# Kernel tuning notes

Measured on AMD Instinct MI355X. Metric: run time of the kernel, lower is better.

The kernel has to match this reference:

```python
import jax, jax.numpy as jnp
import numpy as np

B, S, HID = 1, 2048, 4096
H, HKV = 32, 8
D = HID // H          # 128
G = H // HKV          # 4 query heads per kv head (GQA)


def setup_inputs() -> dict:
    key = jax.random.key(0)
    ks = jax.random.split(key, 5)
    hidden_states = jax.random.normal(ks[0], (B, S, HID), dtype=jnp.float32)
    # additive causal mask: 0 on/below diagonal, large negative above
    causal = jnp.tril(jnp.ones((S, S), dtype=bool))
    attention_mask = jnp.where(causal, 0.0, -1e9).astype(jnp.float32)[None, None]
    sc = 0.02
    wq = jax.random.normal(ks[1], (HID, H * D), dtype=jnp.float32) * sc
    wk = jax.random.normal(ks[2], (HID, HKV * D), dtype=jnp.float32) * sc
    wv = jax.random.normal(ks[3], (HID, HKV * D), dtype=jnp.float32) * sc
    wo = jax.random.normal(ks[4], (H * D, HID), dtype=jnp.float32) * sc
    return {"hidden_states": hidden_states, "attention_mask": attention_mask,
            "wq": wq, "wk": wk, "wv": wv, "wo": wo}


def reference(hidden_states, attention_mask, wq, wk, wv, wo):
    # projections (lora_rank=0 path: plain dense, no bias)
    q = hidden_states @ wq                      # [B,S,H*D]
    k = hidden_states @ wk                      # [B,S,HKV*D]
    v = hidden_states @ wv                      # [B,S,HKV*D]
    # split heads; group query heads by their kv head: head h -> (h//G, h%G)
    q = q.reshape(B, S, HKV, G, D).transpose(0, 2, 3, 1, 4)   # [B,HKV,G,S,D]
    k = k.reshape(B, S, HKV, D).transpose(0, 2, 1, 3)          # [B,HKV,S,D]
    v = v.reshape(B, S, HKV, D).transpose(0, 2, 1, 3)          # [B,HKV,S,D]
    scale = 1.0 / jnp.sqrt(jnp.float32(D))
    # explicit S x S scores (as in source), with GQA kv broadcast over G
    scores = jnp.einsum('bkgsd,bktd->bkgst', q, k) * scale     # [B,HKV,G,S,S]
    scores = scores + attention_mask[:, :, None]               # broadcast over G
    probs = jax.nn.softmax(scores, axis=-1)
    attn = jnp.einsum('bkgst,bktd->bkgsd', probs, v)           # [B,HKV,G,S,D]
    attn = attn.transpose(0, 3, 1, 2, 4).reshape(B, S, H * D)  # [B,S,H*D]
    return attn @ wo                                           # [B,S,HID]
```

## Files before the change

kernel.cpp:

```cpp
#include <hip/hip_runtime.h>
#include <hip/hip_bf16.h>

#define S_LEN 2048
#define HID 4096
#define NH 32
#define NKV 8
#define HD 128
#define LDQKV 6144

typedef __bf16 bf16x8 __attribute__((ext_vector_type(8)));
typedef __bf16 bf16x4 __attribute__((ext_vector_type(4)));
typedef float f32x4 __attribute__((ext_vector_type(4)));

#define GLD16(gp, lp)                                                                   \
    __builtin_amdgcn_global_load_lds((const __attribute__((address_space(1))) void*)(gp), \
                                     (__attribute__((address_space(3))) void*)(lp), 16, 0, 0)

#define MFMA_BF16(a, b, c) __builtin_amdgcn_mfma_f32_16x16x32_bf16((a), (b), (c), 0, 0, 0)

#define SC2_CONST 0.12751743f

__global__ __launch_bounds__(256) void prep_kernel(const float* __restrict__ hs,
                                                   __bf16* __restrict__ Xb,
                                                   const float* __restrict__ wq,
                                                   const float* __restrict__ wk,
                                                   const float* __restrict__ wv,
                                                   __bf16* __restrict__ WqkvT) {
    __shared__ float tile[32][33];
    const int b = blockIdx.x;
    const int tid = threadIdx.x;
    if (b < 8192) {
        int i = (b * 256 + tid) * 4;
        float4 v = *reinterpret_cast<const float4*>(hs + i);
        bf16x4 o;
        o.x = (__bf16)v.x; o.y = (__bf16)v.y; o.z = (__bf16)v.z; o.w = (__bf16)v.w;
        *reinterpret_cast<bf16x4*>(Xb + i) = o;
        return;
    }
    const float* W;
    __bf16* WT;
    int N, bx, by, bb;
    float scale;
    if (b < 24576) {
        bb = b - 8192;  W = wq; WT = WqkvT;                         N = HID;  scale = SC2_CONST;
        bx = bb & 127; by = bb >> 7;
    } else if (b < 28672) {
        bb = b - 24576; W = wk; WT = WqkvT + (size_t)4096 * HID;    N = 1024; scale = 1.0f;
        bx = bb & 31;  by = bb >> 5;
    } else {
        bb = b - 28672; W = wv; WT = WqkvT + (size_t)5120 * HID;    N = 1024; scale = 1.0f;
        bx = bb & 31;  by = bb >> 5;
    }
    const int tx = tid & 31, ty = tid >> 5;
    const int n = bx * 32 + tx;
#pragma unroll
    for (int i = 0; i < 4; i++) {
        int k = by * 32 + ty + i * 8;
        tile[ty + i * 8][tx] = W[(size_t)k * N + n];
    }
    __syncthreads();
    const int k2 = by * 32 + tx;
#pragma unroll
    for (int i = 0; i < 4; i++) {
        int n2 = bx * 32 + ty + i * 8;
        WT[(size_t)n2 * HID + k2] = (__bf16)(tile[tx][ty + i * 8] * scale);
    }
}

__global__ void transpose_cast_kernel(const float* __restrict__ W, __bf16* __restrict__ WT,
                                      int K, int N, float scale) {
    __shared__ float tile[32][33];
    int bx = blockIdx.x;
    int by = blockIdx.y;
    int tx = threadIdx.x;
    int ty = threadIdx.y;
    int n = bx * 32 + tx;
#pragma unroll
    for (int i = 0; i < 4; i++) {
        int k = by * 32 + ty + i * 8;
        tile[ty + i * 8][tx] = W[(size_t)k * N + n];
    }
    __syncthreads();
    int k2 = by * 32 + tx;
#pragma unroll
    for (int i = 0; i < 4; i++) {
        int n2 = bx * 32 + ty + i * 8;
        WT[(size_t)n2 * K + k2] = (__bf16)(tile[tx][ty + i * 8] * scale);
    }
}

__global__ void transpose_bf16_kernel(const __bf16* __restrict__ V, int ldin,
                                      __bf16* __restrict__ VT, int ldout) {
    __shared__ __bf16 tile[32][33];
    int bx = blockIdx.x;
    int by = blockIdx.y;
    int tx = threadIdx.x;
    int ty = threadIdx.y;
#pragma unroll
    for (int i = 0; i < 4; i++)
        tile[ty + i * 8][tx] = V[(size_t)(by * 32 + ty + i * 8) * ldin + bx * 32 + tx];
    __syncthreads();
#pragma unroll
    for (int i = 0; i < 4; i++)
        VT[(size_t)(bx * 32 + ty + i * 8) * ldout + by * 32 + tx] = tile[tx][ty + i * 8];
}

template <int BM, int BN, typename OUT_T>
__global__ __launch_bounds__(256, 2) void gemm_pipe2_kernel(const __bf16* __restrict__ A, int lda,
                                                            const __bf16* __restrict__ BT, int ldb,
                                                            OUT_T* __restrict__ C, int ldc, int K) {
    constexpr int NFA = BM / 32;
    constexpr int NFB = BN / 32;
    constexpr int AR = BM / 32;
    constexpr int BR = BN / 32;
    __shared__ __bf16 As[2][BM * 64];
    __shared__ __bf16 Bs[2][BN * 64];
    const int n0 = blockIdx.x * BN;
    const int m0 = blockIdx.y * BM;
    const int tid = threadIdx.x;
    const int lane = tid & 63, quad = lane >> 4, l16 = lane & 15;
    const int wave = tid >> 6;
    const int wm = (wave >> 1) * (BM / 2);
    const int wn = (wave & 1) * (BN / 2);

    f32x4 acc[NFA][NFB] = {};

    auto STAGE = [&](int b, int kb) {
#pragma unroll
        for (int r = 0; r < AR; r++) {
            int c = r * 256 + tid;
            int row = c >> 3;
            int col8 = (c & 7) ^ (row & 7);
            GLD16(&A[(size_t)(m0 + row) * lda + kb + col8 * 8], &As[b][c * 8]);
        }
#pragma unroll
        for (int r = 0; r < BR; r++) {
            int c = r * 256 + tid;
            int row = c >> 3;
            int col8 = (c & 7) ^ (row & 7);
            GLD16(&BT[(size_t)(n0 + row) * ldb + kb + col8 * 8], &Bs[b][c * 8]);
        }
    };

    auto READ_SET = [&](const __bf16* Asb, const __bf16* Bsb, int kk,
                        bf16x8 (&fa)[NFA], bf16x8 (&fb)[NFB]) {
        int slot = ((kk * 4 + quad) ^ (l16 & 7)) * 8;
#pragma unroll
        for (int i = 0; i < NFA; i++)
            fa[i] = *reinterpret_cast<const bf16x8*>(&Asb[(wm + i * 16 + l16) * 64 + slot]);
#pragma unroll
        for (int j = 0; j < NFB; j++)
            fb[j] = *reinterpret_cast<const bf16x8*>(&Bsb[(wn + j * 16 + l16) * 64 + slot]);
    };

    auto MF = [&](bf16x8 (&fa)[NFA], bf16x8 (&fb)[NFB]) {
        __builtin_amdgcn_s_setprio(1);
#pragma unroll
        for (int i = 0; i < NFA; i++)
#pragma unroll
            for (int j = 0; j < NFB; j++)
                acc[i][j] = MFMA_BF16(fa[i], fb[j], acc[i][j]);
        __builtin_amdgcn_s_setprio(0);
    };

    auto WAIT_SET = [&]() {
        if constexpr (NFA + NFB == 8) {
            asm volatile("s_waitcnt lgkmcnt(8)" ::: "memory");
        } else if constexpr (NFA + NFB == 10) {
            asm volatile("s_waitcnt lgkmcnt(10)" ::: "memory");
        } else {
            asm volatile("s_waitcnt lgkmcnt(12)" ::: "memory");
        }
        __builtin_amdgcn_sched_barrier(0);
    };

    const int nk = K >> 6;
    bf16x8 fa0[NFA], fb0[NFB], fa1[NFA], fb1[NFB];

    STAGE(0, 0);
    STAGE(1, 64);
    if constexpr (AR + BR == 8) {
        asm volatile("s_waitcnt vmcnt(8)" ::: "memory");
    } else {
        asm volatile("s_waitcnt vmcnt(10)" ::: "memory");
    }
    __builtin_amdgcn_sched_barrier(0);
    __builtin_amdgcn_s_barrier();
    READ_SET(As[0], Bs[0], 0, fa0, fb0);

    for (int kt = 0; kt < nk; ++kt) {
        const int cur = kt & 1;
        READ_SET(As[cur], Bs[cur], 1, fa1, fb1);
        WAIT_SET();
        MF(fa0, fb0);
        if (kt + 1 < nk) {
            asm volatile("s_waitcnt vmcnt(0)" ::: "memory");
            __builtin_amdgcn_sched_barrier(0);
            __builtin_amdgcn_s_barrier();
            READ_SET(As[cur ^ 1], Bs[cur ^ 1], 0, fa0, fb0);
            WAIT_SET();
        } else {
            asm volatile("s_waitcnt lgkmcnt(0)" ::: "memory");
            __builtin_amdgcn_sched_barrier(0);
        }
        if (kt + 2 < nk) {
            __builtin_amdgcn_s_barrier();
            STAGE(cur, (kt + 2) << 6);
        }
        MF(fa1, fb1);
    }

#pragma unroll
    for (int i = 0; i < NFA; i++)
#pragma unroll
        for (int j = 0; j < NFB; j++)
#pragma unroll
            for (int r = 0; r < 4; r++) {
                int row = m0 + wm + i * 16 + quad * 4 + r;
                int col = n0 + wn + j * 16 + l16;
                C[(size_t)row * ldc + col] = (OUT_T)acc[i][j][r];
            }
}

__global__ __launch_bounds__(256) void attn_kernel(const __bf16* __restrict__ QKV,
                                                   const __bf16* __restrict__ VT,
                                                   __bf16* __restrict__ Ao,
                                                   __bf16* __restrict__ Opart,
                                                   float* __restrict__ Lp) {
    __shared__ __bf16 Ks[64 * 128];
    __shared__ __bf16 Vs[128 * 64];
    __shared__ __bf16 Pl[4][2][16 * 72];
    int y = 79 - (int)blockIdx.x;
    int qt, c;
    if (y < 8)       { qt = y;                 c = 0; }
    else if (y < 24) { qt = 8 + ((y - 8) >> 1);  c = (y - 8) & 1; }
    else if (y < 48) { qt = 16 + (y - 24) / 3;   c = (y - 24) % 3; }
    else             { qt = 24 + ((y - 48) >> 2); c = (y - 48) & 3; }
    int t0 = c << 3;
    int t1 = min(t0 + 7, qt);
    int hp = blockIdx.y;
    int kvh = hp >> 1;
    int h0 = kvh * 4 + (hp & 1) * 2;
    int tid = threadIdx.x;
    int wave = tid >> 6, lane = tid & 63, quad = lane >> 4, l16 = lane & 15;
    int wq = qt * 64 + wave * 16;
    const __bf16* Kb = QKV + HID + (size_t)kvh * HD;
    const __bf16* Vt = VT + (size_t)kvh * HD * S_LEN;

    bf16x8 qf[2][4];
#pragma unroll
    for (int h = 0; h < 2; h++)
#pragma unroll
        for (int ks = 0; ks < 4; ks++)
            qf[h][ks] = *reinterpret_cast<const bf16x8*>(
                &QKV[(size_t)(wq + l16) * LDQKV + (h0 + h) * HD + ks * 32 + quad * 8]);

    bf16x8 ones;
#pragma unroll
    for (int j = 0; j < 8; j++) ones[j] = (__bf16)1.0f;

    f32x4 acc_o[2][8] = {};
    f32x4 lacc[2] = {};

    bf16x8 kreg[4], vreg[4];
    auto LOADREG = [&](int t) {
        int kv0 = t << 6;
#pragma unroll
        for (int i = 0; i < 4; i++) {
            int cc = i * 256 + tid;
            int row = cc >> 4, sub = cc & 15;
            int col8 = sub ^ (row & 15);
            kreg[i] = *reinterpret_cast<const bf16x8*>(
                &Kb[(size_t)(kv0 + row) * LDQKV + col8 * 8]);
        }
#pragma unroll
        for (int i = 0; i < 4; i++) {
            int cc = i * 256 + tid;
            int row = cc >> 3, sub = cc & 7;
            int col8 = sub ^ (row & 7);
            vreg[i] = *reinterpret_cast<const bf16x8*>(
                &Vt[(size_t)row * S_LEN + kv0 + col8 * 8]);
        }
    };
    auto WRITELDS = [&]() {
#pragma unroll
        for (int i = 0; i < 4; i++)
            *reinterpret_cast<bf16x8*>(&Ks[(i * 256 + tid) * 8]) = kreg[i];
#pragma unroll
        for (int i = 0; i < 4; i++)
            *reinterpret_cast<bf16x8*>(&Vs[(i * 256 + tid) * 8]) = vreg[i];
    };

    LOADREG(t0);
    WRITELDS();
    __syncthreads();

    for (int t = t0; t <= t1; t++) {
        int kv0 = t << 6;
        bool diag = (t == qt);
        if (t < t1) LOADREG(t + 1);

        f32x4 sacc[2][4] = {};
#pragma unroll
        for (int ks = 0; ks < 4; ks++) {
            bf16x8 kf[4];
#pragma unroll
            for (int n = 0; n < 4; n++) {
                int row = n * 16 + l16;
                int sub = (ks * 4 + quad) ^ l16;
                kf[n] = *reinterpret_cast<const bf16x8*>(&Ks[row * 128 + sub * 8]);
            }
#pragma unroll
            for (int n = 0; n < 4; n++) {
                sacc[0][n] = MFMA_BF16(qf[0][ks], kf[n], sacc[0][n]);
                sacc[1][n] = MFMA_BF16(qf[1][ks], kf[n], sacc[1][n]);
            }
        }
#pragma unroll
        for (int h = 0; h < 2; h++) {
            __bf16* Pw = Pl[wave][h];
#pragma unroll
            for (int r = 0; r < 4; r++) {
                int row = wq + quad * 4 + r;
#pragma unroll
                for (int n = 0; n < 4; n++) {
                    float v = sacc[h][n][r];
                    if (diag) {
                        int col = kv0 + n * 16 + l16;
                        if (col > row) v = -1e30f;
                    }
                    Pw[(quad * 4 + r) * 72 + n * 16 + l16] =
                        (__bf16)__builtin_amdgcn_exp2f(v);
                }
            }
        }
#pragma unroll
        for (int ks = 0; ks < 2; ks++) {
            bf16x8 pf0 = *reinterpret_cast<const bf16x8*>(
                &Pl[wave][0][l16 * 72 + ks * 32 + quad * 8]);
            bf16x8 pf1 = *reinterpret_cast<const bf16x8*>(
                &Pl[wave][1][l16 * 72 + ks * 32 + quad * 8]);
            lacc[0] = MFMA_BF16(pf0, ones, lacc[0]);
            lacc[1] = MFMA_BF16(pf1, ones, lacc[1]);
#pragma unroll
            for (int dn = 0; dn < 8; dn++) {
                int row = dn * 16 + l16;
                int sub = (ks * 4 + quad) ^ (row & 7);
                bf16x8 vf = *reinterpret_cast<const bf16x8*>(&Vs[row * 64 + sub * 8]);
                acc_o[0][dn] = MFMA_BF16(pf0, vf, acc_o[0][dn]);
                acc_o[1][dn] = MFMA_BF16(pf1, vf, acc_o[1][dn]);
            }
        }

        __syncthreads();
        if (t < t1) WRITELDS();
        __syncthreads();
    }

    if (qt < 8) {
#pragma unroll
        for (int h = 0; h < 2; h++) {
            float rl[4];
#pragma unroll
            for (int r = 0; r < 4; r++) rl[r] = 1.0f / lacc[h][r];
#pragma unroll
            for (int dn = 0; dn < 8; dn++)
#pragma unroll
                for (int r = 0; r < 4; r++) {
                    int row = wq + quad * 4 + r;
                    int col = (h0 + h) * HD + dn * 16 + l16;
                    Ao[(size_t)row * HID + col] = (__bf16)(acc_o[h][dn][r] * rl[r]);
                }
        }
    } else {
        int sidx = (qt < 16) ? 2 * (qt - 8) + c
                 : (qt < 24) ? 16 + 3 * (qt - 16) + c
                             : 40 + 4 * (qt - 24) + c;
#pragma unroll
        for (int h = 0; h < 2; h++) {
            size_t base = ((size_t)(h0 + h) * 72 + sidx) * 64 + wave * 16;
#pragma unroll
            for (int dn = 0; dn < 8; dn++)
#pragma unroll
                for (int r = 0; r < 4; r++)
                    Opart[(base + quad * 4 + r) * 128 + dn * 16 + l16] =
                        (__bf16)acc_o[h][dn][r];
            if (l16 == 0) {
#pragma unroll
                for (int r = 0; r < 4; r++)
                    Lp[base + quad * 4 + r] = lacc[h][r];
            }
        }
    }
}

__global__ __launch_bounds__(256) void attn_combine(const __bf16* __restrict__ Opart,
                                                    const float* __restrict__ Lp,
                                                    __bf16* __restrict__ Ao) {
    int qt = 8 + (int)blockIdx.x;
    int h = blockIdx.y;
    int tid = threadIdx.x;
    int nch = (qt < 16) ? 2 : (qt < 24) ? 3 : 4;
    int sbase = (qt < 16) ? 2 * (qt - 8)
              : (qt < 24) ? 16 + 3 * (qt - 16)
                          : 40 + 4 * (qt - 24);
    size_t b = ((size_t)h * 72 + sbase) * 64;
#pragma unroll 4
    for (int i = 0; i < 32; i++) {
        int el = i * 256 + tid;
        int rl = el >> 7, col = el & 127;
        float l = 0.0f, O = 0.0f;
        for (int cc = 0; cc < nch; cc++) {
            l += Lp[b + cc * 64 + rl];
            O += (float)Opart[(b + cc * 64 + rl) * 128 + col];
        }
        int row = qt * 64 + rl;
        Ao[(size_t)row * HID + h * HD + col] = (__bf16)(O / l);
    }
}

extern "C" void kernel_launch(void* const* d_in, const int* in_sizes, int n_in,
                              void* d_out, int out_size, void* d_ws, size_t ws_size,
                              hipStream_t stream) {
    const float* hs = (const float*)d_in[0];
    const float* wq = (const float*)d_in[2];
    const float* wk = (const float*)d_in[3];
    const float* wv = (const float*)d_in[4];
    const float* wo = (const float*)d_in[5];
    float* out = (float*)d_out;

    char* ws = (char*)d_ws;
    __bf16* WqkvT = (__bf16*)(ws + (size_t)0);
    __bf16* Opart = (__bf16*)(ws + (size_t)0);
    float*  Lp    = (float*)(ws + ((size_t)40 << 20));
    __bf16* Xb    = (__bf16*)(ws + ((size_t)48 << 20));
    __bf16* QKV   = (__bf16*)(ws + ((size_t)64 << 20));
    __bf16* VTg   = (__bf16*)(ws + ((size_t)88 << 20));
    __bf16* Ab    = Xb;

    prep_kernel<<<32768, 256, 0, stream>>>(hs, Xb, wq, wk, wv, WqkvT);
    gemm_pipe2_kernel<128, 192, __bf16><<<dim3(LDQKV / 192, S_LEN / 128), 256, 0, stream>>>(
        Xb, HID, WqkvT, HID, QKV, LDQKV, HID);
    transpose_bf16_kernel<<<dim3(32, 64), dim3(32, 8), 0, stream>>>(
        QKV + 5120, LDQKV, VTg, S_LEN);
    attn_kernel<<<dim3(80, 16), 256, 0, stream>>>(QKV, VTg, Ab, Opart, Lp);
    attn_combine<<<dim3(24, 32), 256, 0, stream>>>(Opart, Lp, Ab);
    transpose_cast_kernel<<<dim3(128, 128), dim3(32, 8), 0, stream>>>(wo, WqkvT, HID, HID, 1.0f);
    gemm_pipe2_kernel<128, 128, float><<<dim3(HID / 128, S_LEN / 128), 256, 0, stream>>>(
        Ab, HID, WqkvT, HID, out, HID, HID);
}
```

Measured before the change: 508.9 us.

## Process all four GQA heads per block and load K/V via direct-to-LDS loads

The attention kernel now runs 512 threads per block covering all four query heads that share a kv head, so each K/V tile is loaded once per block instead of twice across two blocks. The register-staged prefetch of the next tile is replaced by global_load_lds writes straight into shared memory, bracketed by barriers. This halves K/V global traffic and frees the registers used for staging, but drops the overlap of the next tile's load with compute. It also halves the grid to 640 blocks and raises the launch_bounds occupancy request.

```diff
diff --git a/kernel.cpp b/kernel.cpp
--- a/kernel.cpp
+++ b/kernel.cpp
@@ -222,14 +222,14 @@
             }
 }
 
-__global__ __launch_bounds__(256) void attn_kernel(const __bf16* __restrict__ QKV,
-                                                   const __bf16* __restrict__ VT,
-                                                   __bf16* __restrict__ Ao,
-                                                   __bf16* __restrict__ Opart,
-                                                   float* __restrict__ Lp) {
+__global__ __launch_bounds__(512, 4) void attn_kernel(const __bf16* __restrict__ QKV,
+                                                      const __bf16* __restrict__ VT,
+                                                      __bf16* __restrict__ Ao,
+                                                      __bf16* __restrict__ Opart,
+                                                      float* __restrict__ Lp) {
     __shared__ __bf16 Ks[64 * 128];
     __shared__ __bf16 Vs[128 * 64];
-    __shared__ __bf16 Pl[4][2][16 * 72];
+    __shared__ __bf16 Pl[8][2][16 * 72];
     int y = 79 - (int)blockIdx.x;
     int qt, c;
     if (y < 8)       { qt = y;                 c = 0; }
@@ -238,12 +238,11 @@
     else             { qt = 24 + ((y - 48) >> 2); c = (y - 48) & 3; }
     int t0 = c << 3;
     int t1 = min(t0 + 7, qt);
-    int hp = blockIdx.y;
-    int kvh = hp >> 1;
-    int h0 = kvh * 4 + (hp & 1) * 2;
+    int kvh = blockIdx.y;
     int tid = threadIdx.x;
     int wave = tid >> 6, lane = tid & 63, quad = lane >> 4, l16 = lane & 15;
-    int wq = qt * 64 + wave * 16;
+    int hbase = kvh * 4 + (wave >> 2) * 2;
+    int wq = qt * 64 + (wave & 3) * 16;
     const __bf16* Kb = QKV + HID + (size_t)kvh * HD;
     const __bf16* Vt = VT + (size_t)kvh * HD * S_LEN;
 
@@ -253,7 +252,7 @@
 #pragma unroll
         for (int ks = 0; ks < 4; ks++)
             qf[h][ks] = *reinterpret_cast<const bf16x8*>(
-                &QKV[(size_t)(wq + l16) * LDQKV + (h0 + h) * HD + ks * 32 + quad * 8]);
+                &QKV[(size_t)(wq + l16) * LDQKV + (hbase + h) * HD + ks * 32 + quad * 8]);
 
     bf16x8 ones;
 #pragma unroll
@@ -261,44 +260,26 @@
 
     f32x4 acc_o[2][8] = {};
     f32x4 lacc[2] = {};
-
-    bf16x8 kreg[4], vreg[4];
-    auto LOADREG = [&](int t) {
-        int kv0 = t << 6;
-#pragma unroll
-        for (int i = 0; i < 4; i++) {
-            int cc = i * 256 + tid;
-            int row = cc >> 4, sub = cc & 15;
-            int col8 = sub ^ (row & 15);
-            kreg[i] = *reinterpret_cast<const bf16x8*>(
-                &Kb[(size_t)(kv0 + row) * LDQKV + col8 * 8]);
-        }
-#pragma unroll
-        for (int i = 0; i < 4; i++) {
-            int cc = i * 256 + tid;
-            int row = cc >> 3, sub = cc & 7;
-            int col8 = sub ^ (row & 7);
-            vreg[i] = *reinterpret_cast<const bf16x8*>(
-                &Vt[(size_t)row * S_LEN + kv0 + col8 * 8]);
-        }
-    };
-    auto WRITELDS = [&]() {
-#pragma unroll
-        for (int i = 0; i < 4; i++)
-            *reinterpret_cast<bf16x8*>(&Ks[(i * 256 + tid) * 8]) = kreg[i];
-#pragma unroll
-        for (int i = 0; i < 4; i++)
-            *reinterpret_cast<bf16x8*>(&Vs[(i * 256 + tid) * 8]) = vreg[i];
-    };
-
-    LOADREG(t0);
-    WRITELDS();
-    __syncthreads();
 
     for (int t = t0; t <= t1; t++) {
         int kv0 = t << 6;
         bool diag = (t == qt);
-        if (t < t1) LOADREG(t + 1);
+        __syncthreads();
+#pragma unroll
+        for (int i = 0; i < 2; i++) {
+            int cc = i * 512 + tid;
+            int row = cc >> 4, sub = cc & 15;
+            int col8 = sub ^ (row & 15);
+            GLD16(&Kb[(size_t)(kv0 + row) * LDQKV + col8 * 8], &Ks[cc * 8]);
+        }
+#pragma unroll
+        for (int i = 0; i < 2; i++) {
+            int cc = i * 512 + tid;
+            int row = cc >> 3, sub = cc & 7;
+            int col8 = sub ^ (row & 7);
+            GLD16(&Vt[(size_t)row * S_LEN + kv0 + col8 * 8], &Vs[cc * 8]);
+        }
+        __syncthreads();
 
         f32x4 sacc[2][4] = {};
 #pragma unroll
@@ -351,10 +332,6 @@
                 acc_o[1][dn] = MFMA_BF16(pf1, vf, acc_o[1][dn]);
             }
         }
-
-        __syncthreads();
-        if (t < t1) WRITELDS();
-        __syncthreads();
     }
 
     if (qt < 8) {
@@ -368,7 +345,7 @@
 #pragma unroll
                 for (int r = 0; r < 4; r++) {
                     int row = wq + quad * 4 + r;
-                    int col = (h0 + h) * HD + dn * 16 + l16;
+                    int col = (hbase + h) * HD + dn * 16 + l16;
                     Ao[(size_t)row * HID + col] = (__bf16)(acc_o[h][dn][r] * rl[r]);
                 }
         }
@@ -378,7 +355,7 @@
                              : 40 + 4 * (qt - 24) + c;
 #pragma unroll
         for (int h = 0; h < 2; h++) {
-            size_t base = ((size_t)(h0 + h) * 72 + sidx) * 64 + wave * 16;
+            size_t base = ((size_t)(hbase + h) * 72 + sidx) * 64 + (wave & 3) * 16;
 #pragma unroll
             for (int dn = 0; dn < 8; dn++)
 #pragma unroll
@@ -443,7 +420,7 @@
         Xb, HID, WqkvT, HID, QKV, LDQKV, HID);
     transpose_bf16_kernel<<<dim3(32, 64), dim3(32, 8), 0, stream>>>(
         QKV + 5120, LDQKV, VTg, S_LEN);
-    attn_kernel<<<dim3(80, 16), 256, 0, stream>>>(QKV, VTg, Ab, Opart, Lp);
+    attn_kernel<<<dim3(80, 8), 512, 0, stream>>>(QKV, VTg, Ab, Opart, Lp);
     attn_combine<<<dim3(24, 32), 256, 0, stream>>>(Opart, Lp, Ab);
     transpose_cast_kernel<<<dim3(128, 128), dim3(32, 8), 0, stream>>>(wo, WqkvT, HID, HID, 1.0f);
     gemm_pipe2_kernel<128, 128, float><<<dim3(HID / 128, S_LEN / 128), 256, 0, stream>>>(
```

New measurement: 575.7 us. 13.1% more time.
